# Optimization experiments

Measured on AMD Instinct MI355X. Metric: run time of the kernel, lower is better.

Reference implementation:

```python
import jax, jax.numpy as jnp
import numpy as np

BINS = 256
MAXV = float(2 ** 14 - 1)
LAP_K = jnp.array([[0.0, 1.0, 0.0], [1.0, -4.0, 1.0], [0.0, 1.0, 0.0]], jnp.float32).reshape(1, 1, 3, 3)


def _soft_hist_entropy(flat):
    # flat: (B, N) in arbitrary range; per-image min-max normalize to [0,1]
    fmin = jnp.min(flat, axis=1, keepdims=True)
    fmax = jnp.max(flat, axis=1, keepdims=True)
    rng = fmax - fmin
    rng = jnp.where(rng == 0, jnp.ones_like(rng), rng)
    x = jnp.clip((flat - fmin) / rng, 0.0, 1.0)
    # Triangular soft-histogram weights clamp(1-|x-c_k|/bw, 0) are nonzero for at
    # most the 2 bins adjacent to x, so scatter-add instead of a (B,N,BINS) tensor.
    p = x * BINS - 0.5            # position in bin-center coordinates
    i0 = jnp.floor(p)
    w1 = p - i0                   # weight on bin i0+1
    w0 = 1.0 - w1                 # weight on bin i0
    i0i = i0.astype(jnp.int32)
    i1i = i0i + 1
    v0 = (i0i >= 0) & (i0i < BINS)
    v1 = (i1i >= 0) & (i1i < BINS)

    def hist_one(idx0, idx1, a0, a1, m0, m1):
        h = jnp.zeros((BINS,), flat.dtype)
        h = h.at[jnp.clip(idx0, 0, BINS - 1)].add(jnp.where(m0, a0, 0.0))
        h = h.at[jnp.clip(idx1, 0, BINS - 1)].add(jnp.where(m1, a1, 0.0))
        return h

    hist = jax.vmap(hist_one)(i0i, i1i, w0, w1, v0, v1)  # (B, BINS)
    hist = hist / (jnp.sum(hist, axis=1, keepdims=True) + 1e-10)
    ent = -jnp.sum(hist * jnp.log2(hist + 1e-10), axis=1)
    return ent / jnp.float32(np.log2(BINS))


def _extract_features(image):
    # normalize 14-bit input to [0,1] iff values exceed 1 (matches torch branch)
    image = jnp.where(jnp.max(image) > 1.0, image / MAXV, image)
    B = image.shape[0]
    flat = image.reshape(B, -1)
    variance = jnp.var(flat, axis=1, ddof=1)   # torch.var is unbiased
    mn = jnp.min(flat, axis=1)
    mx = jnp.max(flat, axis=1)
    ent = _soft_hist_entropy(flat)
    lap = jax.lax.conv_general_dilated(
        image, LAP_K, window_strides=(1, 1), padding=[(1, 1), (1, 1)],
        dimension_numbers=('NCHW', 'OIHW', 'NCHW'))
    lap_var = jnp.var(lap.reshape(B, -1), axis=1, ddof=1)
    return jnp.stack([variance, mn, mx, ent, lap_var], axis=1)  # (B, 5)


def setup_inputs() -> dict:
    key = jax.random.key(0)
    ks = jax.random.split(key, 4)
    image = jax.random.uniform(ks[0], (16, 1, 1024, 1280), jnp.float32) * MAXV
    # Kaiming normal fan_in (relu): std = sqrt(2 / fan_in); biases zero
    W1 = jax.random.normal(ks[1], (64, 5), jnp.float32) * np.float32(np.sqrt(2.0 / 5))
    W2 = jax.random.normal(ks[2], (64, 64), jnp.float32) * np.float32(np.sqrt(2.0 / 64))
    W3 = jax.random.normal(ks[3], (3, 64), jnp.float32) * np.float32(np.sqrt(2.0 / 64))
    return {
        'image': image,
        'W1': W1, 'b1': jnp.zeros((64,), jnp.float32),
        'W2': W2, 'b2': jnp.zeros((64,), jnp.float32),
        'W3': W3, 'b3': jnp.zeros((3,), jnp.float32),
    }


def reference(image, W1, b1, W2, b2, W3, b3):
    feats = _extract_features(image)                       # (B, 5)
    h = jax.nn.relu(feats @ W1.T + b1)
    h = jax.nn.relu(h @ W2.T + b2)
    logits = h @ W3.T + b3                                  # (B, 3)
    probs = jax.nn.softmax(logits, axis=1)
    class_ids = jnp.argmax(probs, axis=1)
    return class_ids, probs, feats
```

## Files before the change

### kernel.cpp

```cpp
#include <hip/hip_runtime.h>
#include <cfloat>
#include <math.h>

#define IMG_B 16
#define IMG_H 1024
#define IMG_W 1280
#define NPIX (IMG_H * IMG_W)
#define BINS 256
#define SLICES 64
#define NBLK (IMG_B * SLICES)
#define F4_PER_SLICE (16 * IMG_W / 4)
#define FIXP 65536.0f

__device__ __forceinline__ unsigned encf(float f) {
    unsigned u = __float_as_uint(f);
    return (u >> 31) ? ~u : (u | 0x80000000u);
}
__device__ __forceinline__ float decf(unsigned u) {
    unsigned b = (u & 0x80000000u) ? (u & 0x7fffffffu) : ~u;
    return __uint_as_float(b);
}


__global__ __launch_bounds__(256) void k_minmax(const float* __restrict__ img,
                                                uint2* __restrict__ mmp) {
    const int blk = blockIdx.x;
    const int tid = threadIdx.x;
    const float4* p = (const float4*)img + (size_t)blk * F4_PER_SLICE;

    float fmn = FLT_MAX, fmx = -FLT_MAX;
    #pragma unroll 4
    for (int i = tid; i < F4_PER_SLICE; i += 256) {
        float4 v = p[i];
        fmn = fminf(fmn, fminf(fminf(v.x, v.y), fminf(v.z, v.w)));
        fmx = fmaxf(fmx, fmaxf(fmaxf(v.x, v.y), fmaxf(v.z, v.w)));
    }
    for (int o = 32; o; o >>= 1) {
        fmn = fminf(fmn, __shfl_down(fmn, (unsigned)o, 64));
        fmx = fmaxf(fmx, __shfl_down(fmx, (unsigned)o, 64));
    }
    __shared__ float rmn[4], rmx[4];
    int lane = tid & 63, wv = tid >> 6;
    if (lane == 0) { rmn[wv] = fmn; rmx[wv] = fmx; }
    __syncthreads();
    if (tid == 0) {
        float mn = fminf(fminf(rmn[0], rmn[1]), fminf(rmn[2], rmn[3]));
        float mx = fmaxf(fmaxf(rmx[0], rmx[1]), fmaxf(rmx[2], rmx[3]));
        mmp[blk] = make_uint2(encf(mn), encf(mx));
    }
}

__global__ __launch_bounds__(256) void k_main(const float* __restrict__ img,
                                              const uint2* __restrict__ mmp,
                                              double* __restrict__ mom,
                                              unsigned* __restrict__ bhist) {
    const int blk = blockIdx.x;
    const int tid = threadIdx.x;
    const int b   = blk >> 6;
    const int sl  = blk & 63;
    const int lane = tid & 63, wv = tid >> 6;

    __shared__ unsigned lh[BINS];
    __shared__ float sh_mm[2];
    __shared__ float swred[4][4];

    if (tid < 64) {
        uint2 e = mmp[b * 64 + tid];
        unsigned emn = e.x, emx = e.y;
        for (int o = 32; o; o >>= 1) {
            emn = min(emn, (unsigned)__shfl_down(emn, (unsigned)o, 64));
            emx = max(emx, (unsigned)__shfl_down(emx, (unsigned)o, 64));
        }
        if (tid == 0) { sh_mm[0] = decf(emn); sh_mm[1] = decf(emx); }
    }
    lh[tid] = 0u;
    __syncthreads();

    const float fmn = sh_mm[0], fmx = sh_mm[1];
    float rng = fmx - fmn;
    if (rng == 0.f) rng = 1.f;
    const float inv = 1.f / rng;

    const float* base = img + (size_t)b * NPIX;
    const int r0 = sl * 16;

    float fs = 0.f, fs2 = 0.f, fls = 0.f, fls2 = 0.f;

    #pragma unroll 2
    for (int k = 0; k < 20; ++k) {
        int i   = tid + k * 256;
        int ri  = i / 320;
        int c   = i - ri * 320;
        int r   = r0 + ri;
        const float* rowf = base + (size_t)r * IMG_W;
        float4 m = ((const float4*)rowf)[c];
        float4 up = make_float4(0.f, 0.f, 0.f, 0.f);
        float4 dn = make_float4(0.f, 0.f, 0.f, 0.f);
        if (r > 0)          up = ((const float4*)(rowf - IMG_W))[c];
        if (r < IMG_H - 1)  dn = ((const float4*)(rowf + IMG_W))[c];
        float lft = (c > 0)   ? rowf[4 * c - 1] : 0.f;
        float rgt = (c < 319) ? rowf[4 * c + 4] : 0.f;

        fs  += (m.x + m.y) + (m.z + m.w);
        fs2 += (m.x * m.x + m.y * m.y) + (m.z * m.z + m.w * m.w);

        float l0 = up.x + dn.x + lft + m.y - 4.f * m.x;
        float l1 = up.y + dn.y + m.x + m.z - 4.f * m.y;
        float l2 = up.z + dn.z + m.y + m.w - 4.f * m.z;
        float l3 = up.w + dn.w + m.z + rgt - 4.f * m.w;
        fls  += (l0 + l1) + (l2 + l3);
        fls2 += (l0 * l0 + l1 * l1) + (l2 * l2 + l3 * l3);

        #pragma unroll
        for (int j = 0; j < 4; ++j) {
            float vv = (j == 0) ? m.x : (j == 1) ? m.y : (j == 2) ? m.z : m.w;
            float x  = fminf(fmaxf((vv - fmn) * inv, 0.f), 1.f);
            float pp = x * 256.f - 0.5f;
            float fi = floorf(pp);
            int   i0 = (int)fi;
            float w1 = pp - fi;
            unsigned w1q = (unsigned)(w1 * FIXP + 0.5f);
            unsigned w0q = 65536u - w1q;
            if (i0 >= 0)        atomicAdd(&lh[i0], w0q);
            if (i0 < BINS - 1)  atomicAdd(&lh[i0 + 1], w1q);
        }
    }

    for (int o = 32; o; o >>= 1) {
        fs   += __shfl_down(fs,   (unsigned)o, 64);
        fs2  += __shfl_down(fs2,  (unsigned)o, 64);
        fls  += __shfl_down(fls,  (unsigned)o, 64);
        fls2 += __shfl_down(fls2, (unsigned)o, 64);
    }
    if (lane == 0) {
        swred[0][wv] = fs;  swred[1][wv] = fs2;
        swred[2][wv] = fls; swred[3][wv] = fls2;
    }
    __syncthreads();
    if (tid == 0) {
        double S  = (double)swred[0][0] + (double)swred[0][1] + (double)swred[0][2] + (double)swred[0][3];
        double S2 = (double)swred[1][0] + (double)swred[1][1] + (double)swred[1][2] + (double)swred[1][3];
        double LS  = (double)swred[2][0] + (double)swred[2][1] + (double)swred[2][2] + (double)swred[2][3];
        double LS2 = (double)swred[3][0] + (double)swred[3][1] + (double)swred[3][2] + (double)swred[3][3];
        mom[blk * 4 + 0] = S;  mom[blk * 4 + 1] = S2;
        mom[blk * 4 + 2] = LS; mom[blk * 4 + 3] = LS2;
    }
    bhist[blk * BINS + tid] = lh[tid];
}

__global__ __launch_bounds__(256) void k_final(
    const unsigned* __restrict__ bhist, const double* __restrict__ mom,
    const uint2* __restrict__ mmp,
    const float* __restrict__ W1, const float* __restrict__ b1,
    const float* __restrict__ W2, const float* __restrict__ b2,
    const float* __restrict__ W3, const float* __restrict__ b3,
    float* __restrict__ out)
{
    const int ib = blockIdx.x;
    const int tid = threadIdx.x;
    const int lane = tid & 63, wv = tid >> 6;

    __shared__ double dred[4];
    __shared__ float  fred[4];
    __shared__ double smom[4];
    __shared__ unsigned smm2[2];
    __shared__ unsigned sgm[4];
    __shared__ float f5[5], h1[64], h2[64], lg[3];

    double h = 0.0;
    for (int s = 0; s < 64; ++s)
        h += (double)bhist[(ib * 64 + s) * BINS + tid];

    double tot = h;
    for (int o = 32; o; o >>= 1) tot += __shfl_down(tot, (unsigned)o, 64);
    if (lane == 0) dred[wv] = tot;
    __syncthreads();
    tot = dred[0] + dred[1] + dred[2] + dred[3];

    double hv = h * (1.0 / 65536.0);
    double tv = tot * (1.0 / 65536.0);
    float hn = (float)(hv / (tv + 1e-10));
    float ce = hn * log2f(hn + 1e-10f);
    for (int o = 32; o; o >>= 1) ce += __shfl_down(ce, (unsigned)o, 64);
    if (lane == 0) fred[wv] = ce;

    if (tid < 64) {
        double q0 = mom[(ib * 64 + tid) * 4 + 0];
        double q1 = mom[(ib * 64 + tid) * 4 + 1];
        double q2 = mom[(ib * 64 + tid) * 4 + 2];
        double q3 = mom[(ib * 64 + tid) * 4 + 3];
        uint2 e = mmp[ib * 64 + tid];
        unsigned emn = e.x, emx = e.y;
        for (int o = 32; o; o >>= 1) {
            q0 += __shfl_down(q0, (unsigned)o, 64);
            q1 += __shfl_down(q1, (unsigned)o, 64);
            q2 += __shfl_down(q2, (unsigned)o, 64);
            q3 += __shfl_down(q3, (unsigned)o, 64);
            emn = min(emn, (unsigned)__shfl_down(emn, (unsigned)o, 64));
            emx = max(emx, (unsigned)__shfl_down(emx, (unsigned)o, 64));
        }
        if (tid == 0) {
            smom[0] = q0; smom[1] = q1; smom[2] = q2; smom[3] = q3;
            smm2[0] = emn; smm2[1] = emx;
        }
    }
    {
        unsigned g = max(max(mmp[tid].y, mmp[256 + tid].y),
                         max(mmp[512 + tid].y, mmp[768 + tid].y));
        for (int o = 32; o; o >>= 1)
            g = max(g, (unsigned)__shfl_down(g, (unsigned)o, 64));
        if (lane == 0) sgm[wv] = g;
    }
    __syncthreads();

    if (tid == 0) {
        float ent = -(fred[0] + fred[1] + fred[2] + fred[3]) / 8.f;
        float gmax = decf(max(max(sgm[0], sgm[1]), max(sgm[2], sgm[3])));
        float sc = (gmax > 1.f) ? (1.f / 16383.f) : 1.f;
        double N = (double)NPIX;
        double S = smom[0], S2 = smom[1], LS = smom[2], LS2 = smom[3];
        double sc2 = (double)sc * (double)sc;
        float var  = (float)((S2  - S  * S  / N) / (N - 1.0) * sc2);
        float lvar = (float)((LS2 - LS * LS / N) / (N - 1.0) * sc2);
        float mn = decf(smm2[0]) * sc;
        float mx = decf(smm2[1]) * sc;
        float* fo = out + 64 + ib * 5;
        fo[0] = var; fo[1] = mn; fo[2] = mx; fo[3] = ent; fo[4] = lvar;
        f5[0] = var; f5[1] = mn; f5[2] = mx; f5[3] = ent; f5[4] = lvar;
    }
    __syncthreads();

    if (tid < 64) {
        float a = b1[tid];
        #pragma unroll
        for (int k = 0; k < 5; ++k) a += W1[tid * 5 + k] * f5[k];
        h1[tid] = fmaxf(a, 0.f);
    }
    __syncthreads();
    if (tid < 64) {
        float a2 = b2[tid];
        #pragma unroll
        for (int k = 0; k < 64; ++k) a2 += W2[tid * 64 + k] * h1[k];
        h2[tid] = fmaxf(a2, 0.f);
    }
    __syncthreads();
    if (tid < 3) {
        float a3 = b3[tid];
        #pragma unroll
        for (int k = 0; k < 64; ++k) a3 += W3[tid * 64 + k] * h2[k];
        lg[tid] = a3;
    }
    __syncthreads();
    if (tid == 0) {
        float m = fmaxf(lg[0], fmaxf(lg[1], lg[2]));
        float e0 = expf(lg[0] - m), e1 = expf(lg[1] - m), e2 = expf(lg[2] - m);
        float inv = 1.f / (e0 + e1 + e2);
        float p0 = e0 * inv, p1 = e1 * inv, p2 = e2 * inv;
        out[16 + ib * 3 + 0] = p0;
        out[16 + ib * 3 + 1] = p1;
        out[16 + ib * 3 + 2] = p2;
        int cid = 0; float bm = p0;
        if (p1 > bm) { bm = p1; cid = 1; }
        if (p2 > bm) { bm = p2; cid = 2; }
        out[ib] = (float)cid;
    }
}

extern "C" void kernel_launch(void* const* d_in, const int* in_sizes, int n_in,
                              void* d_out, int out_size, void* d_ws, size_t ws_size,
                              hipStream_t stream) {
    const float* img = (const float*)d_in[0];
    const float* W1  = (const float*)d_in[1];
    const float* b1  = (const float*)d_in[2];
    const float* W2  = (const float*)d_in[3];
    const float* b2  = (const float*)d_in[4];
    const float* W3  = (const float*)d_in[5];
    const float* b3  = (const float*)d_in[6];
    float* out = (float*)d_out;

    char* ws = (char*)d_ws;
    uint2*    mmp   = (uint2*)ws;
    double*   mom   = (double*)(ws + 8192);
    unsigned* bhist = (unsigned*)(ws + 40960);

    k_minmax<<<NBLK, 256, 0, stream>>>(img, mmp);
    k_main  <<<NBLK, 256, 0, stream>>>(img, mmp, mom, bhist);
    k_final <<<IMG_B, 256, 0, stream>>>(bhist, mom, mmp,
                                        W1, b1, W2, b2, W3, b3, out);
}
```

Baseline: 159.5 us.

## Fuse min/max into moments pass and halve histogram atomics via packed 64-bit bins

Moves the per-slice min/max reduction into the stencil/moments kernel, and gives the histogram its own kernel that reads only the centre pixels. Each pixel now performs a single 64-bit LDS atomic that packs a count in the high word and the upper-bin weight in the low word. Per-bin values are reconstructed afterwards from adjacent entries. This removes one of the two atomics per pixel and separates the atomic-heavy work from the stencil work, so neither kernel is held back by the other. The cost is wider 64-bit LDS atomics and a rewritten affine clamp, which could shift edge-bin rounding slightly.

New measurement: 158.1 us (median of 2 runs). No clear change (-0.8%).

```diff
diff --git a/kernel.cpp b/kernel.cpp
--- a/kernel.cpp
+++ b/kernel.cpp
@@ -10,7 +10,6 @@
 #define SLICES 64
 #define NBLK (IMG_B * SLICES)
 #define F4_PER_SLICE (16 * IMG_W / 4)
-#define FIXP 65536.0f
 
 __device__ __forceinline__ unsigned encf(float f) {
     unsigned u = __float_as_uint(f);
@@ -22,69 +21,20 @@
 }
 
 
-__global__ __launch_bounds__(256) void k_minmax(const float* __restrict__ img,
-                                                uint2* __restrict__ mmp) {
-    const int blk = blockIdx.x;
-    const int tid = threadIdx.x;
-    const float4* p = (const float4*)img + (size_t)blk * F4_PER_SLICE;
-
-    float fmn = FLT_MAX, fmx = -FLT_MAX;
-    #pragma unroll 4
-    for (int i = tid; i < F4_PER_SLICE; i += 256) {
-        float4 v = p[i];
-        fmn = fminf(fmn, fminf(fminf(v.x, v.y), fminf(v.z, v.w)));
-        fmx = fmaxf(fmx, fmaxf(fmaxf(v.x, v.y), fmaxf(v.z, v.w)));
-    }
-    for (int o = 32; o; o >>= 1) {
-        fmn = fminf(fmn, __shfl_down(fmn, (unsigned)o, 64));
-        fmx = fmaxf(fmx, __shfl_down(fmx, (unsigned)o, 64));
-    }
-    __shared__ float rmn[4], rmx[4];
-    int lane = tid & 63, wv = tid >> 6;
-    if (lane == 0) { rmn[wv] = fmn; rmx[wv] = fmx; }
-    __syncthreads();
-    if (tid == 0) {
-        float mn = fminf(fminf(rmn[0], rmn[1]), fminf(rmn[2], rmn[3]));
-        float mx = fmaxf(fmaxf(rmx[0], rmx[1]), fmaxf(rmx[2], rmx[3]));
-        mmp[blk] = make_uint2(encf(mn), encf(mx));
-    }
-}
-
-__global__ __launch_bounds__(256) void k_main(const float* __restrict__ img,
-                                              const uint2* __restrict__ mmp,
-                                              double* __restrict__ mom,
-                                              unsigned* __restrict__ bhist) {
+__global__ __launch_bounds__(256) void k_pre(const float* __restrict__ img,
+                                             uint2* __restrict__ mmp,
+                                             double* __restrict__ mom) {
     const int blk = blockIdx.x;
     const int tid = threadIdx.x;
     const int b   = blk >> 6;
     const int sl  = blk & 63;
     const int lane = tid & 63, wv = tid >> 6;
 
-    __shared__ unsigned lh[BINS];
-    __shared__ float sh_mm[2];
-    __shared__ float swred[4][4];
-
-    if (tid < 64) {
-        uint2 e = mmp[b * 64 + tid];
-        unsigned emn = e.x, emx = e.y;
-        for (int o = 32; o; o >>= 1) {
-            emn = min(emn, (unsigned)__shfl_down(emn, (unsigned)o, 64));
-            emx = max(emx, (unsigned)__shfl_down(emx, (unsigned)o, 64));
-        }
-        if (tid == 0) { sh_mm[0] = decf(emn); sh_mm[1] = decf(emx); }
-    }
-    lh[tid] = 0u;
-    __syncthreads();
-
-    const float fmn = sh_mm[0], fmx = sh_mm[1];
-    float rng = fmx - fmn;
-    if (rng == 0.f) rng = 1.f;
-    const float inv = 1.f / rng;
-
     const float* base = img + (size_t)b * NPIX;
     const int r0 = sl * 16;
 
     float fs = 0.f, fs2 = 0.f, fls = 0.f, fls2 = 0.f;
+    float fmn = FLT_MAX, fmx = -FLT_MAX;
 
     #pragma unroll 2
     for (int k = 0; k < 20; ++k) {
@@ -103,6 +53,8 @@
 
         fs  += (m.x + m.y) + (m.z + m.w);
         fs2 += (m.x * m.x + m.y * m.y) + (m.z * m.z + m.w * m.w);
+        fmn = fminf(fmn, fminf(fminf(m.x, m.y), fminf(m.z, m.w)));
+        fmx = fmaxf(fmx, fmaxf(fmaxf(m.x, m.y), fmaxf(m.z, m.w)));
 
         float l0 = up.x + dn.x + lft + m.y - 4.f * m.x;
         float l1 = up.y + dn.y + m.x + m.z - 4.f * m.y;
@@ -110,20 +62,6 @@
         float l3 = up.w + dn.w + m.z + rgt - 4.f * m.w;
         fls  += (l0 + l1) + (l2 + l3);
         fls2 += (l0 * l0 + l1 * l1) + (l2 * l2 + l3 * l3);
-
-        #pragma unroll
-        for (int j = 0; j < 4; ++j) {
-            float vv = (j == 0) ? m.x : (j == 1) ? m.y : (j == 2) ? m.z : m.w;
-            float x  = fminf(fmaxf((vv - fmn) * inv, 0.f), 1.f);
-            float pp = x * 256.f - 0.5f;
-            float fi = floorf(pp);
-            int   i0 = (int)fi;
-            float w1 = pp - fi;
-            unsigned w1q = (unsigned)(w1 * FIXP + 0.5f);
-            unsigned w0q = 65536u - w1q;
-            if (i0 >= 0)        atomicAdd(&lh[i0], w0q);
-            if (i0 < BINS - 1)  atomicAdd(&lh[i0 + 1], w1q);
-        }
     }
 
     for (int o = 32; o; o >>= 1) {
@@ -131,21 +69,82 @@
         fs2  += __shfl_down(fs2,  (unsigned)o, 64);
         fls  += __shfl_down(fls,  (unsigned)o, 64);
         fls2 += __shfl_down(fls2, (unsigned)o, 64);
-    }
+        fmn = fminf(fmn, __shfl_down(fmn, (unsigned)o, 64));
+        fmx = fmaxf(fmx, __shfl_down(fmx, (unsigned)o, 64));
+    }
+    __shared__ float swred[4][4];
+    __shared__ float rmn[4], rmx[4];
     if (lane == 0) {
         swred[0][wv] = fs;  swred[1][wv] = fs2;
         swred[2][wv] = fls; swred[3][wv] = fls2;
+        rmn[wv] = fmn; rmx[wv] = fmx;
     }
     __syncthreads();
     if (tid == 0) {
-        double S  = (double)swred[0][0] + (double)swred[0][1] + (double)swred[0][2] + (double)swred[0][3];
-        double S2 = (double)swred[1][0] + (double)swred[1][1] + (double)swred[1][2] + (double)swred[1][3];
+        double S   = (double)swred[0][0] + (double)swred[0][1] + (double)swred[0][2] + (double)swred[0][3];
+        double S2  = (double)swred[1][0] + (double)swred[1][1] + (double)swred[1][2] + (double)swred[1][3];
         double LS  = (double)swred[2][0] + (double)swred[2][1] + (double)swred[2][2] + (double)swred[2][3];
         double LS2 = (double)swred[3][0] + (double)swred[3][1] + (double)swred[3][2] + (double)swred[3][3];
         mom[blk * 4 + 0] = S;  mom[blk * 4 + 1] = S2;
         mom[blk * 4 + 2] = LS; mom[blk * 4 + 3] = LS2;
-    }
-    bhist[blk * BINS + tid] = lh[tid];
+        float mn = fminf(fminf(rmn[0], rmn[1]), fminf(rmn[2], rmn[3]));
+        float mx = fmaxf(fmaxf(rmx[0], rmx[1]), fmaxf(rmx[2], rmx[3]));
+        mmp[blk] = make_uint2(encf(mn), encf(mx));
+    }
+}
+
+__global__ __launch_bounds__(256) void k_hist(const float* __restrict__ img,
+                                              const uint2* __restrict__ mmp,
+                                              unsigned* __restrict__ bhist) {
+    const int blk = blockIdx.x;
+    const int tid = threadIdx.x;
+    const int b   = blk >> 6;
+
+    __shared__ unsigned long long lh64[BINS + 1];
+    __shared__ float sh_ab[2];
+
+    if (tid < 64) {
+        uint2 e = mmp[b * 64 + tid];
+        unsigned emn = e.x, emx = e.y;
+        for (int o = 32; o; o >>= 1) {
+            emn = min(emn, (unsigned)__shfl_down(emn, (unsigned)o, 64));
+            emx = max(emx, (unsigned)__shfl_down(emx, (unsigned)o, 64));
+        }
+        if (tid == 0) {
+            float fmn = decf(emn), fmx = decf(emx);
+            float rng = fmx - fmn;
+            if (rng == 0.f) rng = 1.f;
+            float a = 256.f / rng;
+            float bb = -fmn * a - 0.5f;
+            sh_ab[0] = a; sh_ab[1] = bb;
+        }
+    }
+    lh64[tid] = 0ull;
+    if (tid == 0) lh64[BINS] = 0ull;
+    __syncthreads();
+
+    const float a = sh_ab[0], bb = sh_ab[1];
+
+    const float4* p = (const float4*)img + (size_t)blk * F4_PER_SLICE;
+    #pragma unroll 2
+    for (int k = 0; k < 20; ++k) {
+        float4 v = p[tid + k * 256];
+        #pragma unroll
+        for (int j = 0; j < 4; ++j) {
+            float vv = (j == 0) ? v.x : (j == 1) ? v.y : (j == 2) ? v.z : v.w;
+            float pp = fminf(fmaxf(vv * a + bb, -0.5f), 255.5f);
+            float fi = floorf(pp);
+            int   i0 = (int)fi;
+            unsigned w1q = (unsigned)((pp - fi) * 65536.f + 0.5f);
+            atomicAdd(&lh64[i0 + 1], 0x100000000ull + (unsigned long long)w1q);
+        }
+    }
+    __syncthreads();
+
+    unsigned long long a0 = lh64[tid];
+    unsigned long long a1 = lh64[tid + 1];
+    unsigned long long h  = ((a1 >> 32) << 16) - (a1 & 0xffffffffull) + (a0 & 0xffffffffull);
+    bhist[blk * BINS + tid] = (unsigned)h;
 }
 
 __global__ __launch_bounds__(256) void k_final(
@@ -231,10 +230,10 @@
     __syncthreads();
 
     if (tid < 64) {
-        float a = b1[tid];
-        #pragma unroll
-        for (int k = 0; k < 5; ++k) a += W1[tid * 5 + k] * f5[k];
-        h1[tid] = fmaxf(a, 0.f);
+        float aa = b1[tid];
+        #pragma unroll
+        for (int k = 0; k < 5; ++k) aa += W1[tid * 5 + k] * f5[k];
+        h1[tid] = fmaxf(aa, 0.f);
     }
     __syncthreads();
     if (tid < 64) {
@@ -283,8 +282,8 @@
     double*   mom   = (double*)(ws + 8192);
     unsigned* bhist = (unsigned*)(ws + 40960);
 
-    k_minmax<<<NBLK, 256, 0, stream>>>(img, mmp);
-    k_main  <<<NBLK, 256, 0, stream>>>(img, mmp, mom, bhist);
-    k_final <<<IMG_B, 256, 0, stream>>>(bhist, mom, mmp,
-                                        W1, b1, W2, b2, W3, b3, out);
-}
+    k_pre  <<<NBLK, 256, 0, stream>>>(img, mmp, mom);
+    k_hist <<<NBLK, 256, 0, stream>>>(img, mmp, bhist);
+    k_final<<<IMG_B, 256, 0, stream>>>(bhist, mom, mmp,
+                                       W1, b1, W2, b2, W3, b3, out);
+}
```
